# Performance work log

Hardware: AMD Instinct MI355X
Metric: run time of the kernel (lower is better)

The kernel has to match this reference:

```python
import jax, jax.numpy as jnp
import numpy as np

B, NS, NI, UP = 1024, 64, 64, 4
H = 256


def setup_inputs() -> dict:
    key = jax.random.key(0)
    ks = list(jax.random.split(key, 40))
    it = iter(ks)
    def lin(din, dout):
        return (jax.random.normal(next(it), (din, dout), jnp.float32) / np.sqrt(din)).astype(jnp.float32)
    d = {}
    d['rays_o'] = jax.random.normal(next(it), (B, 3), jnp.float32) * 0.1
    rd = jax.random.normal(next(it), (B, 3), jnp.float32)
    d['rays_d'] = rd / jnp.linalg.norm(rd, axis=-1, keepdims=True)
    d['near'] = jnp.full((B, 1), 0.5, jnp.float32)
    d['far'] = jnp.full((B, 1), 2.5, jnp.float32)
    d['W_sdf0'] = lin(3, H); d['b_sdf0'] = jnp.zeros((H,), jnp.float32)
    d['W_sdf1'] = lin(H, H); d['b_sdf1'] = jnp.zeros((H,), jnp.float32)
    d['W_sdf2'] = lin(H, 1 + H); d['b_sdf2'] = jnp.zeros((1 + H,), jnp.float32)
    d['s_var'] = jnp.asarray(0.3, jnp.float32)
    d['Wc0'] = lin(9 + H, H); d['bc0'] = jnp.zeros((H,), jnp.float32)
    d['Wc1'] = lin(H, 3); d['bc1'] = jnp.zeros((3,), jnp.float32)
    d['Wn0'] = lin(6, H); d['bn0'] = jnp.zeros((H,), jnp.float32)
    d['Wn1'] = lin(H, H); d['bn1'] = jnp.zeros((H,), jnp.float32)
    d['Wn2'] = lin(H, 4); d['bn2'] = jnp.zeros((4,), jnp.float32)
    d['Wrf0'] = lin(3, H); d['brf0'] = jnp.zeros((H,), jnp.float32)
    d['Wrf1'] = lin(H, 1); d['brf1'] = jnp.zeros((1,), jnp.float32)
    d['Wrl0'] = lin(3, H); d['brl0'] = jnp.zeros((H,), jnp.float32)
    d['Wrl1'] = lin(H, 1); d['brl1'] = jnp.zeros((1,), jnp.float32)
    d['Wnm0'] = lin(H, 128); d['bnm0'] = jnp.zeros((128,), jnp.float32)
    d['Wnm1'] = lin(128, 3); d['bnm1'] = jnp.zeros((3,), jnp.float32)
    return d


def _forward(args):
    (rays_o, rays_d, near, far, W_sdf0, b_sdf0, W_sdf1, b_sdf1, W_sdf2, b_sdf2,
     s_var, Wc0, bc0, Wc1, bc1, Wn0, bn0, Wn1, bn1, Wn2, bn2,
     Wrf0, brf0, Wrf1, brf1, Wrl0, brl0, Wrl1, brl1, Wnm0, bnm0, Wnm1, bnm1) = args
    relu, sig = jax.nn.relu, jax.nn.sigmoid
    Bn = rays_o.shape[0]
    inv_s = jnp.clip(jnp.exp(10.0 * s_var), 1e-6, 1e6)  # SingleVarianceNetwork
    sample_dist = 2.0 / NS

    def sdf_out(p):
        h = relu(p @ W_sdf0 + b_sdf0)
        h = relu(h @ W_sdf1 + b_sdf1)
        return h @ W_sdf2 + b_sdf2  # [N, 1+256]: sdf + feature

    def sdf_val(p):
        return sdf_out(p)[..., 0]

    def sample_pdf(bins, weights, n):  # deterministic (perturb=False)
        w = weights + 1e-5
        pdf = w / jnp.sum(w, -1, keepdims=True)
        cdf = jnp.concatenate([jnp.zeros_like(pdf[:, :1]), jnp.cumsum(pdf, -1)], -1)
        u = jnp.broadcast_to(jnp.linspace(0.5 / n, 1.0 - 0.5 / n, n, dtype=bins.dtype), (bins.shape[0], n))
        inds = jax.vmap(lambda c, uu: jnp.searchsorted(c, uu, side='right'))(cdf, u)
        below = jnp.clip(inds - 1, 0, bins.shape[-1] - 1)
        above = jnp.clip(inds, 0, bins.shape[-1] - 1)
        cb = jnp.take_along_axis(cdf, below, -1); ca = jnp.take_along_axis(cdf, above, -1)
        bb = jnp.take_along_axis(bins, below, -1); ba = jnp.take_along_axis(bins, above, -1)
        denom = jnp.where(ca - cb < 1e-5, 1.0, ca - cb)
        return bb + (u - cb) / denom * (ba - bb)

    def up_sample(o, d, z, sdf, n_imp, s):  # NeuS hierarchical SDF upsampling
        pts = o[:, None, :] + d[:, None, :] * z[..., None]
        radius = jnp.linalg.norm(pts, axis=-1)
        inside = ((radius[:, :-1] < 1.0) | (radius[:, 1:] < 1.0)).astype(z.dtype)
        prev_sdf, next_sdf = sdf[:, :-1], sdf[:, 1:]
        prev_z, next_z = z[:, :-1], z[:, 1:]
        mid_sdf = 0.5 * (prev_sdf + next_sdf)
        cos_val = (next_sdf - prev_sdf) / (next_z - prev_z + 1e-5)
        prev_cos = jnp.concatenate([jnp.zeros_like(cos_val[:, :1]), cos_val[:, :-1]], -1)
        cos_val = jnp.clip(jnp.minimum(cos_val, prev_cos), -1e3, 0.0) * inside
        dist = next_z - prev_z
        pc = sig((mid_sdf - 0.5 * cos_val * dist) * s)
        nc = sig((mid_sdf + 0.5 * cos_val * dist) * s)
        alpha = (pc - nc + 1e-5) / (pc + 1e-5)
        trans = jnp.cumprod(jnp.concatenate([jnp.ones_like(alpha[:, :1]), 1.0 - alpha + 1e-7], -1), -1)[:, :-1]
        return sample_pdf(z, alpha * trans, n_imp)

    def importance_sdf(o, d):
        z = near + (far - near) * jnp.linspace(0.0, 1.0, NS)[None, :]
        sdf = sdf_val((o[:, None, :] + d[:, None, :] * z[..., None]).reshape(-1, 3)).reshape(Bn, -1)
        for i in range(UP):
            nz = up_sample(o, d, z, sdf, NI // UP, 64.0 * 2 ** i)
            z = jnp.sort(jnp.concatenate([z, nz], -1), -1)
            if i + 1 < UP:
                sdf = sdf_val((o[:, None, :] + d[:, None, :] * z[..., None]).reshape(-1, 3)).reshape(Bn, -1)
        return jax.lax.stop_gradient(z)  # sampler runs under no_grad

    def render_sdf(o, d, z):  # rendering_rays_SDF (NeuS)
        S = z.shape[1]
        dists = jnp.concatenate([z[:, 1:] - z[:, :-1], jnp.full_like(z[:, :1], sample_dist)], -1)
        mid_z = z + 0.5 * dists
        pts = (o[:, None, :] + d[:, None, :] * mid_z[..., None]).reshape(-1, 3)
        dirs = jnp.broadcast_to(d[:, None, :], (Bn, S, 3)).reshape(-1, 3)
        out = sdf_out(pts)
        sdf = out[:, :1]; feat = out[:, 1:]
        grads = jax.grad(lambda p: jnp.sum(sdf_val(p)))(pts)  # analytic SDF gradient
        true_cos = jnp.sum(dirs * grads, -1, keepdims=True)
        iter_cos = -relu(-true_cos)  # cos_anneal_ratio = 1.0
        df = dists.reshape(-1, 1)
        pc = sig((sdf - 0.5 * iter_cos * df) * inv_s)
        nc = sig((sdf + 0.5 * iter_cos * df) * inv_s)
        alpha = jnp.clip((pc - nc + 1e-5) / (pc + 1e-5), 0.0, 1.0).reshape(Bn, S)
        trans = jnp.cumprod(jnp.concatenate([jnp.ones_like(alpha[:, :1]), 1.0 - alpha + 1e-7], -1), -1)[:, :-1]
        w = alpha * trans
        depths = jax.lax.stop_gradient(jnp.sum(mid_z * w, -1, keepdims=True))  # AlphaBlend depth, no_grad
        nrm = grads / (jnp.linalg.norm(grads, axis=-1, keepdims=True) + 1e-12)  # NormalizedAnalytic
        cin = jnp.concatenate([pts, nrm, dirs, feat], -1)  # color_d_in=9 + 256 feat
        rgb = sig(relu(cin @ Wc0 + bc0) @ Wc1 + bc1).reshape(Bn, S, 3)
        color = jnp.sum(rgb * w[..., None], 1)
        smooth = ((feat @ Wnm0 + bnm0) @ Wnm1 + bnm1).reshape(Bn, S, 3)  # Linear->Linear, no act
        surf_n = jnp.sum(w[..., None] * nrm.reshape(Bn, S, 3), 1)
        surf_n = surf_n / (jnp.linalg.norm(surf_n, axis=-1, keepdims=True) + 1e-12)
        return color, w, depths, surf_n, smooth

    def nerf_eval(pts, dirs):
        h = relu(jnp.concatenate([pts, dirs], -1) @ Wn0 + bn0)
        h = relu(h @ Wn1 + bn1)
        o = h @ Wn2 + bn2
        return o[:, 0], sig(o[:, 1:4])

    def mask_prob(pts, Wa, ba, Wb, bb):  # Refract/ReflectNetwork, d_in=3 d_out=1
        return sig((relu(pts @ Wa + ba) @ Wb + bb)[:, 0])

    def importance_nerf(o, d, z, n_imp):
        S = z.shape[1]
        dists = jnp.concatenate([z[:, 1:] - z[:, :-1], jnp.full_like(z[:, :1], 1e10)], -1)
        pts = (o[:, None, :] + d[:, None, :] * z[..., None]).reshape(-1, 3)
        dirs = jnp.broadcast_to(d[:, None, :], (Bn, S, 3)).reshape(-1, 3)
        sigma, _ = nerf_eval(pts, dirs)
        alpha = 1.0 - jnp.exp(-relu(sigma).reshape(Bn, S) * dists)
        trans = jnp.cumprod(jnp.concatenate([jnp.ones_like(alpha[:, :1]), 1.0 - alpha + 1e-7], -1), -1)[:, :-1]
        w = alpha * trans
        nz = sample_pdf(z, w[:, :-1], n_imp)
        return jax.lax.stop_gradient(jnp.sort(jnp.concatenate([z, nz], -1), -1))

    def render_nerf(o, d, z):
        S = z.shape[1]
        dists = jnp.concatenate([z[:, 1:] - z[:, :-1], jnp.full_like(z[:, :1], sample_dist)], -1)
        mid_z = z + 0.5 * dists
        pts = (o[:, None, :] + d[:, None, :] * mid_z[..., None]).reshape(-1, 3)
        dirs = jnp.broadcast_to(d[:, None, :], (Bn, S, 3)).reshape(-1, 3)
        sigma, rgb = nerf_eval(pts, dirs)
        alpha = 1.0 - jnp.exp(-relu(sigma).reshape(Bn, S) * dists)
        trans = jnp.cumprod(jnp.concatenate([jnp.ones_like(alpha[:, :1]), 1.0 - alpha + 1e-7], -1), -1)[:, :-1]
        w = alpha * trans
        color = jnp.sum(rgb.reshape(Bn, S, 3) * w[..., None], 1)
        m1 = jnp.sum(w * mask_prob(pts, Wrf0, brf0, Wrf1, brf1).reshape(Bn, S), -1, keepdims=True)
        m2 = jnp.sum(w * mask_prob(pts, Wrl0, brl0, Wrl1, brl1).reshape(Bn, S), -1, keepdims=True)
        return color, m1, m2

    # ---- main pipeline (eval: perturb=False, geometry_warmup_state=False) ----
    z_sdf = importance_sdf(rays_o, rays_d)
    _color_sdf, _w_sdf, depths, surf_n, _smooth = render_sdf(rays_o, rays_d, z_sdf)

    z0 = near + (far - near) * jnp.linspace(0.0, 1.0, NS)[None, :]
    z1 = importance_nerf(rays_o, rays_d, z0, NI)
    c1, m1, m2 = render_nerf(rays_o, rays_d, z1)

    # hit point + reflect/refract directions
    hit = rays_o + rays_d * depths
    n = surf_n
    cos = jnp.sum(rays_d * n, -1, keepdims=True)
    n = jnp.where(cos > 0, -n, n)  # face the incoming ray
    cosi = -jnp.sum(rays_d * n, -1, keepdims=True)
    refl = rays_d + 2.0 * cosi * n
    eta = 1.0 / 1.5
    k = 1.0 - eta * eta * (1.0 - cosi * cosi)
    refr = eta * rays_d + (eta * cosi - jnp.sqrt(jnp.maximum(k, 0.0))) * n
    refr = jnp.where(k < 0, refl, refr)  # total internal reflection
    refl = refl / (jnp.linalg.norm(refl, axis=-1, keepdims=True) + 1e-12)
    refr = refr / (jnp.linalg.norm(refr, axis=-1, keepdims=True) + 1e-12)

    ones = jnp.ones((Bn, 1), z1.dtype)
    # reflect (fanshe) pass: near=0.05 far=3.7
    zf0 = 0.05 * ones + (3.7 - 0.05) * jnp.linspace(0.0, 1.0, NS)[None, :]
    zf = importance_nerf(hit, refl, zf0, NI)
    cf, _, _ = render_nerf(hit, refl, zf)
    # refract (zheshe) passes: (0,3.7) and (0.5,3.7) with half samples
    zz0 = 3.7 * jnp.linspace(0.0, 1.0, NS // 2)[None, :] * ones
    zz = importance_nerf(hit, refr, zz0, NI // 2)
    cz, _, _ = render_nerf(hit, refr, zz)
    zb0 = 0.5 * ones + (3.7 - 0.5) * jnp.linspace(0.0, 1.0, NS // 2)[None, :]
    zb = importance_nerf(hit, refr, zb0, NI // 2)
    cb_, _, _ = render_nerf(hit, refr, zb)
    rgb_z = 0.5 * cz + 0.5 * cb_

    rgb = c1 * (1.0 - m2) + cf * m2
    rgb = rgb * (1.0 - m1) + rgb_z * m1
    return rgb


def reference(rays_o, rays_d, near, far, W_sdf0, b_sdf0, W_sdf1, b_sdf1, W_sdf2, b_sdf2,
              s_var, Wc0, bc0, Wc1, bc1, Wn0, bn0, Wn1, bn1, Wn2, bn2,
              Wrf0, brf0, Wrf1, brf1, Wrl0, brl0, Wrl1, brl1, Wnm0, bnm0, Wnm1, bnm1):
    return _forward((rays_o, rays_d, near, far, W_sdf0, b_sdf0, W_sdf1, b_sdf1, W_sdf2, b_sdf2,
                     s_var, Wc0, bc0, Wc1, bc1, Wn0, bn0, Wn1, bn1, Wn2, bn2,
                     Wrf0, brf0, Wrf1, brf1, Wrl0, brl0, Wrl1, brl1, Wnm0, bnm0, Wnm1, bnm1))
```

## Files before the change

kernel.cpp:

```cpp
#include <hip/hip_runtime.h>

#define NB 1024
#define HH 256
#define ZS 128
#define PP 16
#define SAMPLE_DIST 0.03125f

typedef __attribute__((ext_vector_type(8))) _Float16 half8v;
typedef __attribute__((ext_vector_type(4))) float f32x4;

struct ZInit { int on; const float* loA; const float* hiA; float lo0,hi0,lo1,hi1; };

__device__ __forceinline__ float sigm(float x){ return 1.0f/(1.0f+__expf(-x)); }

__device__ __forceinline__ float iscan_prod(float v, int lane){
  #pragma unroll
  for (int o=1;o<64;o<<=1){ float u=__shfl_up(v,o); if(lane>=o) v*=u; }
  return v;
}
__device__ __forceinline__ float iscan_sum(float v, int lane){
  #pragma unroll
  for (int o=1;o<64;o<<=1){ float u=__shfl_up(v,o); if(lane>=o) v+=u; }
  return v;
}
__device__ __forceinline__ float wave_sum(float v){
  #pragma unroll
  for (int o=1;o<64;o<<=1) v += __shfl_xor(v,o);
  return v;
}

__device__ __forceinline__ void load_point2(const float* __restrict__ o, const float* __restrict__ dv,
    const float* __restrict__ z, int idx, int S, int midflag, int zst, ZInit zi, float* pt, float* dir)
{
  int r = idx / S;
  int i = idx - r*S;
  float zz;
  if (zi.on){
    float a=zi.loA[r], b=zi.hiA[r];
    zz = a + (b-a)*((float)i/(float)(S-1));
    if (midflag){
      float z1 = a + (b-a)*((float)(i+1)/(float)(S-1));
      zz = (i < S-1) ? 0.5f*(zz+z1) : (zz + 0.5f*SAMPLE_DIST);
    }
  } else {
    const float* zr = z + r*zst;
    zz = zr[i];
    if (midflag) zz = (i < S-1) ? 0.5f*(zz + zr[i+1]) : (zz + 0.5f*SAMPLE_DIST);
  }
  #pragma unroll
  for (int c=0;c<3;c++){
    float dc = dv[r*3+c];
    pt[c] = o[r*3+c] + dc*zz;
    if (dir) dir[c] = dc;
  }
}

__device__ __forceinline__ void load_point(const float* __restrict__ o, const float* __restrict__ dv,
    const float* __restrict__ z, int idx, int S, int midflag, float* pt, float* dir)
{
  int r = idx / S;
  int i = idx - r*S;
  const float* zr = z + r*ZS;
  float zz = zr[i];
  if (midflag) zz = (i < S-1) ? 0.5f*(zz + zr[i+1]) : (zz + 0.5f*SAMPLE_DIST);
  #pragma unroll
  for (int c=0;c<3;c++){
    float dc = dv[r*3+c];
    pt[c] = o[r*3+c] + dc*zz;
    if (dir) dir[c] = dc;
  }
}

__global__ __launch_bounds__(256) void prep_kernel(const float* __restrict__ W1, const float* __restrict__ W2,
    float* __restrict__ W1T, float* __restrict__ w2col)
{
  int idx = blockIdx.x*256 + threadIdx.x;
  int j = idx >> 8, k = idx & 255;
  W1T[j*HH + k] = W1[k*HH + j];
  if (idx < HH) w2col[idx] = W2[idx*257];
}

__global__ __launch_bounds__(256) void prep_bfrag_kernel(const float* __restrict__ W1,
    short* __restrict__ Bh)
{
  int idx = blockIdx.x*256 + threadIdx.x;
  int j = idx & 7;
  int lane = (idx>>3) & 63;
  int s = (idx>>9) & 7;
  int nt = idx >> 12;
  int k = s*32 + ((lane>>4)<<3) + j;
  int n = nt*16 + (lane&15);
  union { _Float16 h; short s; } u;
  u.h = (_Float16)W1[k*256 + n];
  Bh[idx] = u.s;
}

__global__ void build_rays_kernel(const float* __restrict__ ro, const float* __restrict__ rd,
    const float* __restrict__ nearA, const float* __restrict__ farA,
    const float* __restrict__ hit, const float* __restrict__ refl, const float* __restrict__ refr,
    float* __restrict__ rO, float* __restrict__ rD, float* __restrict__ rLo, float* __restrict__ rHi)
{
  int r = blockIdx.x*256 + threadIdx.x;
  if (r >= 4096) return;
  int m = r>>10, q = r&1023;
  const float* so; const float* sd; float lo,hi;
  if (m==0){ so=ro+q*3; sd=rd+q*3; lo=nearA[q]; hi=farA[q]; }
  else if (m==1){ so=hit+q*3; sd=refl+q*3; lo=0.05f; hi=3.7f; }
  else if (m==2){ so=hit+q*3; sd=refr+q*3; lo=0.f; hi=3.7f; }
  else { so=hit+q*3; sd=refr+q*3; lo=0.5f; hi=3.7f; }
  rO[r*3]=so[0]; rO[r*3+1]=so[1]; rO[r*3+2]=so[2];
  rD[r*3]=sd[0]; rD[r*3+1]=sd[1]; rD[r*3+2]=sd[2];
  rLo[r]=lo; rHi[r]=hi;
}

__global__ __launch_bounds__(256) void sdf_mfma_kernel(
    const float* __restrict__ o, const float* __restrict__ dv, const float* __restrict__ z,
    int S, int midflag, int zst, ZInit zi,
    const float* __restrict__ W0, const float* __restrict__ b0,
    const short* __restrict__ Bh, const float* __restrict__ b1,
    const float* __restrict__ w2col, const float* __restrict__ b2,
    float* __restrict__ out_sdf, unsigned short* __restrict__ signs)
{
  __shared__ float xs[128][5];
  __shared__ float w0s[3*HH];
  __shared__ float b0s[HH];
  int t = threadIdx.x;
  int base = blockIdx.x*128;
  for (int i=t;i<3*HH;i+=256) w0s[i]=W0[i];
  b0s[t]=b0[t];
  if (t<128){
    float pt[3];
    load_point2(o,dv,z,base+t,S,midflag,zst,zi,pt,nullptr);
    xs[t][0]=pt[0]; xs[t][1]=pt[1]; xs[t][2]=pt[2];
  }
  __syncthreads();
  int wave=t>>6, lane=t&63, g=lane>>4, c16=lane&15;
  half8v af[2][8];
  #pragma unroll
  for (int mt=0;mt<2;mt++){
    const float* xp = xs[wave*32 + mt*16 + c16];
    float x0=xp[0],x1=xp[1],x2=xp[2];
    #pragma unroll
    for (int s8=0;s8<8;s8++){
      int nb = s8*32 + g*8;
      union { _Float16 h[8]; half8v v; } uh;
      #pragma unroll
      for (int j=0;j<8;j++){
        int n=nb+j;
        float a=b0s[n];
        a=fmaf(x0,w0s[n],a);
        a=fmaf(x1,w0s[HH+n],a);
        a=fmaf(x2,w0s[2*HH+n],a);
        uh.h[j]=(_Float16)fmaxf(a,0.f);
      }
      af[mt][s8]=uh.v;
    }
  }
  float pacc[2][4];
  #pragma unroll
  for (int mt=0;mt<2;mt++){ pacc[mt][0]=0.f; pacc[mt][1]=0.f; pacc[mt][2]=0.f; pacc[mt][3]=0.f; }
  for (int ntp=0;ntp<8;ntp++){
    int nt0=2*ntp;
    f32x4 aH[2][2];
    #pragma unroll
    for (int mt=0;mt<2;mt++)
      #pragma unroll
      for (int h=0;h<2;h++) aH[mt][h]=(f32x4){0.f,0.f,0.f,0.f};
    const short* b0h = Bh + nt0*4096 + lane*8;
    #pragma unroll
    for (int s8=0;s8<8;s8++){
      half8v bh0 = *(const half8v*)(b0h + s8*512);
      half8v bh1 = *(const half8v*)(b0h + 4096 + s8*512);
      #pragma unroll
      for (int mt=0;mt<2;mt++){
        aH[mt][0] = __builtin_amdgcn_mfma_f32_16x16x32_f16(af[mt][s8], bh0, aH[mt][0], 0,0,0);
        aH[mt][1] = __builtin_amdgcn_mfma_f32_16x16x32_f16(af[mt][s8], bh1, aH[mt][1], 0,0,0);
      }
    }
    #pragma unroll
    for (int h=0;h<2;h++){
      int nt = nt0+h;
      int n = nt*16 + c16;
      float b1v = b1[n];
      float wv = w2col[n];
      #pragma unroll
      for (int mt=0;mt<2;mt++){
        f32x4 acc = aH[mt][h];
        #pragma unroll
        for (int rr=0;rr<4;rr++){
          float hv = acc[rr]+b1v;
          if (signs){
            unsigned long long m0 = __ballot(hv>0.f);
            if (c16==0) signs[(base+wave*32+mt*16+g*4+rr)*16+nt] = (unsigned short)(m0>>(16*g));
          }
          pacc[mt][rr]=fmaf(fmaxf(hv,0.f),wv,pacc[mt][rr]);
        }
      }
    }
  }
  #pragma unroll
  for (int mt=0;mt<2;mt++)
    #pragma unroll
    for (int rr=0;rr<4;rr++){
      float v=pacc[mt][rr];
      v+=__shfl_xor(v,1); v+=__shfl_xor(v,2); v+=__shfl_xor(v,4); v+=__shfl_xor(v,8);
      pacc[mt][rr]=v;
    }
  if (c16==0){
    float bb2=b2[0];
    #pragma unroll
    for (int mt=0;mt<2;mt++)
      #pragma unroll
      for (int rr=0;rr<4;rr++)
        out_sdf[base + wave*32 + mt*16 + g*4 + rr] = pacc[mt][rr] + bb2;
  }
}

__global__ __launch_bounds__(256) void sdf_bwd_mfma_kernel(
    const float* __restrict__ o, const float* __restrict__ dv, const float* __restrict__ z,
    const float* __restrict__ W0, const float* __restrict__ b0,
    const unsigned short* __restrict__ signs,
    const short* __restrict__ Th,
    const float* __restrict__ w2col,
    float* __restrict__ out_grad)
{
  __shared__ float xs[128][5];
  __shared__ float w0s[3*HH];
  __shared__ float b0s[HH];
  __shared__ _Float16 w2h_s[HH];
  int t = threadIdx.x;
  int base = blockIdx.x*128;
  for (int i=t;i<3*HH;i+=256) w0s[i]=W0[i];
  b0s[t]=b0[t];
  w2h_s[t]=(_Float16)w2col[t];
  if (t<128){
    float pt[3];
    ZInit zn{0,nullptr,nullptr,0,0,0,0};
    load_point2(o,dv,z,base+t,128,1,ZS,zn,pt,nullptr);
    xs[t][0]=pt[0]; xs[t][1]=pt[1]; xs[t][2]=pt[2];
  }
  __syncthreads();
  int wave=t>>6, lane=t&63, g=lane>>4, c16=lane&15;
  half8v af[2][8];
  #pragma unroll
  for (int mt=0;mt<2;mt++){
    int ptA = base + wave*32 + mt*16 + c16;
    #pragma unroll
    for (int s8=0;s8<8;s8++){
      int j0 = s8*32 + g*8;
      unsigned short wch = signs[ptA*16 + (j0>>4)];
      unsigned bits = ((unsigned)wch >> ((g&1)*8)) & 0xFFu;
      union { _Float16 h[8]; half8v v; } uh;
      #pragma unroll
      for (int jj=0;jj<8;jj++){
        bool on = (bits>>jj)&1u;
        uh.h[jj] = on ? w2h_s[j0+jj] : (_Float16)0.f;
      }
      af[mt][s8]=uh.v;
    }
  }
  float acc3[2][4][3];
  #pragma unroll
  for (int mt=0;mt<2;mt++)
    #pragma unroll
    for (int rr=0;rr<4;rr++){ acc3[mt][rr][0]=0.f; acc3[mt][rr][1]=0.f; acc3[mt][rr][2]=0.f; }
  for (int ntp=0;ntp<8;ntp++){
    int nt0=2*ntp;
    f32x4 aH[2][2];
    #pragma unroll
    for (int mt=0;mt<2;mt++)
      #pragma unroll
      for (int h=0;h<2;h++) aH[mt][h]=(f32x4){0.f,0.f,0.f,0.f};
    const short* b0h = Th + nt0*4096 + lane*8;
    #pragma unroll
    for (int s8=0;s8<8;s8++){
      half8v bh0 = *(const half8v*)(b0h + s8*512);
      half8v bh1 = *(const half8v*)(b0h + 4096 + s8*512);
      #pragma unroll
      for (int mt=0;mt<2;mt++){
        aH[mt][0] = __builtin_amdgcn_mfma_f32_16x16x32_f16(af[mt][s8], bh0, aH[mt][0], 0,0,0);
        aH[mt][1] = __builtin_amdgcn_mfma_f32_16x16x32_f16(af[mt][s8], bh1, aH[mt][1], 0,0,0);
      }
    }
    #pragma unroll
    for (int h=0;h<2;h++){
      int nt = nt0+h;
      int tn = nt*16 + c16;
      float w0a=w0s[tn], w0b=w0s[HH+tn], w0c=w0s[2*HH+tn], bb=b0s[tn];
      #pragma unroll
      for (int mt=0;mt<2;mt++){
        f32x4 acc = aH[mt][h];
        #pragma unroll
        for (int rr=0;rr<4;rr++){
          const float* xq = xs[wave*32 + mt*16 + g*4 + rr];
          float h0 = fmaf(xq[0],w0a, fmaf(xq[1],w0b, fmaf(xq[2],w0c, bb)));
          float dh0 = (h0>0.f) ? acc[rr] : 0.f;
          acc3[mt][rr][0]=fmaf(dh0,w0a,acc3[mt][rr][0]);
          acc3[mt][rr][1]=fmaf(dh0,w0b,acc3[mt][rr][1]);
          acc3[mt][rr][2]=fmaf(dh0,w0c,acc3[mt][rr][2]);
        }
      }
    }
  }
  #pragma unroll
  for (int mt=0;mt<2;mt++)
    #pragma unroll
    for (int rr=0;rr<4;rr++)
      #pragma unroll
      for (int cc=0;cc<3;cc++){
        float v=acc3[mt][rr][cc];
        v+=__shfl_xor(v,1); v+=__shfl_xor(v,2); v+=__shfl_xor(v,4); v+=__shfl_xor(v,8);
        acc3[mt][rr][cc]=v;
      }
  if (c16==0){
    #pragma unroll
    for (int mt=0;mt<2;mt++)
      #pragma unroll
      for (int rr=0;rr<4;rr++){
        int pt_ = base + wave*32 + mt*16 + g*4 + rr;
        out_grad[pt_*3+0]=acc3[mt][rr][0];
        out_grad[pt_*3+1]=acc3[mt][rr][1];
        out_grad[pt_*3+2]=acc3[mt][rr][2];
      }
  }
}

__global__ __launch_bounds__(256) void nerf_mfma_batch(
    const float* __restrict__ rO, const float* __restrict__ rD,
    const float* __restrict__ rLo, const float* __restrict__ rHi,
    const float* __restrict__ zbuf, int ptsA, int SA, int SB, int NRA, int useZ, int midflag,
    const float* __restrict__ W0, const float* __restrict__ b0,
    const short* __restrict__ Bh, const float* __restrict__ b1,
    const float* __restrict__ W2, const float* __restrict__ b2,
    float* __restrict__ out_sigma, float* __restrict__ out_rgb)
{
  __shared__ float xs[128][9];
  __shared__ float w0s[6*HH];
  __shared__ float b0s[HH];
  int t = threadIdx.x;
  int base = blockIdx.x*128;
  int wave=t>>6, lane=t&63, g=lane>>4, c16=lane&15;
  for (int i=t;i<6*HH;i+=256) w0s[i]=W0[i];
  b0s[t]=b0[t];
  if (t<128){
    int idx=base+t;
    int r,i,S;
    if (idx<ptsA){ S=SA; r=idx/SA; i=idx-r*SA; }
    else { int q=idx-ptsA; S=SB; r=NRA+q/SB; i=q-(q/SB)*SB; }
    float zz;
    if (!useZ){
      float a=rLo[r], b=rHi[r];
      zz = a + (b-a)*((float)i/(float)(S-1));
      if (midflag){
        float z1 = a + (b-a)*((float)(i+1)/(float)(S-1));
        zz = (i<S-1)? 0.5f*(zz+z1) : (zz+0.5f*SAMPLE_DIST);
      }
    } else {
      const float* zr = zbuf + r*128;
      zz = zr[i];
      if (midflag) zz = (i<S-1)? 0.5f*(zz+zr[i+1]) : (zz+0.5f*SAMPLE_DIST);
    }
    #pragma unroll
    for (int c=0;c<3;c++){
      float dc=rD[r*3+c];
      xs[t][c]   = rO[r*3+c] + dc*zz;
      xs[t][3+c] = dc;
    }
  }
  __syncthreads();
  half8v af[2][8];
  #pragma unroll
  for (int mt=0;mt<2;mt++){
    const float* xp = xs[wave*32 + mt*16 + c16];
    float x0=xp[0],x1=xp[1],x2=xp[2],x3=xp[3],x4=xp[4],x5=xp[5];
    #pragma unroll
    for (int s8=0;s8<8;s8++){
      int nb = s8*32 + g*8;
      union { _Float16 h[8]; half8v v; } uh;
      #pragma unroll
      for (int j=0;j<8;j++){
        int n=nb+j;
        float a=b0s[n];
        a=fmaf(x0,w0s[n],a);
        a=fmaf(x1,w0s[HH+n],a);
        a=fmaf(x2,w0s[2*HH+n],a);
        a=fmaf(x3,w0s[3*HH+n],a);
        a=fmaf(x4,w0s[4*HH+n],a);
        a=fmaf(x5,w0s[5*HH+n],a);
        uh.h[j]=(_Float16)fmaxf(a,0.f);
      }
      af[mt][s8]=uh.v;
    }
  }
  float pacc[2][4][4];
  #pragma unroll
  for (int mt=0;mt<2;mt++)
    #pragma unroll
    for (int rr=0;rr<4;rr++){ pacc[mt][rr][0]=0.f; pacc[mt][rr][1]=0.f; pacc[mt][rr][2]=0.f; pacc[mt][rr][3]=0.f; }
  for (int ntp=0;ntp<8;ntp++){
    int nt0=2*ntp;
    f32x4 aH[2][2];
    #pragma unroll
    for (int mt=0;mt<2;mt++)
      #pragma unroll
      for (int h=0;h<2;h++) aH[mt][h]=(f32x4){0.f,0.f,0.f,0.f};
    const short* b0h = Bh + nt0*4096 + lane*8;
    #pragma unroll
    for (int s8=0;s8<8;s8++){
      half8v bh0 = *(const half8v*)(b0h + s8*512);
      half8v bh1 = *(const half8v*)(b0h + 4096 + s8*512);
      #pragma unroll
      for (int mt=0;mt<2;mt++){
        aH[mt][0] = __builtin_amdgcn_mfma_f32_16x16x32_f16(af[mt][s8], bh0, aH[mt][0], 0,0,0);
        aH[mt][1] = __builtin_amdgcn_mfma_f32_16x16x32_f16(af[mt][s8], bh1, aH[mt][1], 0,0,0);
      }
    }
    #pragma unroll
    for (int h=0;h<2;h++){
      int nt = nt0+h;
      int n = nt*16 + c16;
      float b1v = b1[n];
      float4 w2v = *(const float4*)(W2 + n*4);
      #pragma unroll
      for (int mt=0;mt<2;mt++){
        f32x4 acc = aH[mt][h];
        #pragma unroll
        for (int rr=0;rr<4;rr++){
          float hh = fmaxf(acc[rr]+b1v, 0.f);
          pacc[mt][rr][0]=fmaf(hh,w2v.x,pacc[mt][rr][0]);
          pacc[mt][rr][1]=fmaf(hh,w2v.y,pacc[mt][rr][1]);
          pacc[mt][rr][2]=fmaf(hh,w2v.z,pacc[mt][rr][2]);
          pacc[mt][rr][3]=fmaf(hh,w2v.w,pacc[mt][rr][3]);
        }
      }
    }
  }
  #pragma unroll
  for (int mt=0;mt<2;mt++)
    #pragma unroll
    for (int rr=0;rr<4;rr++)
      #pragma unroll
      for (int c=0;c<4;c++){
        float v=pacc[mt][rr][c];
        v+=__shfl_xor(v,1); v+=__shfl_xor(v,2); v+=__shfl_xor(v,4); v+=__shfl_xor(v,8);
        pacc[mt][rr][c]=v;
      }
  if (c16==0){
    float bb0=b2[0], bb1=b2[1], bb2v=b2[2], bb3=b2[3];
    #pragma unroll
    for (int mt=0;mt<2;mt++)
      #pragma unroll
      for (int rr=0;rr<4;rr++){
        int pt_ = base + wave*32 + mt*16 + g*4 + rr;
        out_sigma[pt_] = pacc[mt][rr][0] + bb0;
        out_rgb[pt_*3+0] = sigm(pacc[mt][rr][1] + bb1);
        out_rgb[pt_*3+1] = sigm(pacc[mt][rr][2] + bb2v);
        out_rgb[pt_*3+2] = sigm(pacc[mt][rr][3] + bb3);
      }
  }
}

__global__ __launch_bounds__(256) void mask_kernel(
    const float* __restrict__ o, const float* __restrict__ dv, const float* __restrict__ z, int S,
    const float* __restrict__ Wa0, const float* __restrict__ ba0, const float* __restrict__ Wa1, const float* __restrict__ ba1,
    const float* __restrict__ Wb0, const float* __restrict__ bb0, const float* __restrict__ Wb1, const float* __restrict__ bb1,
    float* __restrict__ outA, float* __restrict__ outB)
{
  __shared__ __align__(16) float hA[PP][HH];
  __shared__ float pin[PP][4];
  __shared__ float part[PP][16];
  int t=threadIdx.x;
  int base=blockIdx.x*PP;
  if (t<PP){
    float pt[3];
    load_point(o,dv,z,base+t,S,1,pt,nullptr);
    pin[t][0]=pt[0]; pin[t][1]=pt[1]; pin[t][2]=pt[2];
  }
  __syncthreads();
  {
    float w0=Wa0[t], w1=Wa0[HH+t], w2=Wa0[2*HH+t], bb=ba0[t];
    #pragma unroll
    for (int p=0;p<PP;p++){
      float v = fmaf(pin[p][0],w0, fmaf(pin[p][1],w1, fmaf(pin[p][2],w2, bb)));
      hA[p][t]=fmaxf(v,0.f);
    }
  }
  __syncthreads();
  {
    int p=t>>4, g=t&15;
    float s=0.f;
    #pragma unroll
    for (int m=0;m<16;m++){ int j=g+16*m; s=fmaf(hA[p][j], Wa1[j], s); }
    part[p][g]=s;
  }
  __syncthreads();
  if (t<PP){
    float s=ba1[0];
    #pragma unroll
    for (int g=0;g<16;g++) s+=part[t][g];
    outA[base+t]=sigm(s);
  }
  __syncthreads();
  {
    float w0=Wb0[t], w1=Wb0[HH+t], w2=Wb0[2*HH+t], bb=bb0[t];
    #pragma unroll
    for (int p=0;p<PP;p++){
      float v = fmaf(pin[p][0],w0, fmaf(pin[p][1],w1, fmaf(pin[p][2],w2, bb)));
      hA[p][t]=fmaxf(v,0.f);
    }
  }
  __syncthreads();
  {
    int p=t>>4, g=t&15;
    float s=0.f;
    #pragma unroll
    for (int m=0;m<16;m++){ int j=g+16*m; s=fmaf(hA[p][j], Wb1[j], s); }
    part[p][g]=s;
  }
  __syncthreads();
  if (t<PP){
    float s=bb1[0];
    #pragma unroll
    for (int g=0;g<16;g++) s+=part[t][g];
    outB[base+t]=sigm(s);
  }
}

__global__ __launch_bounds__(256) void upsample_wave_kernel(float* __restrict__ z,
    const float* __restrict__ sdf, const float* __restrict__ o, const float* __restrict__ dv,
    int S, float s, ZInit zi)
{
  __shared__ float zsh[4][128], ssh[4][128], csh[4][128], nzsh[4][16];
  int wave=threadIdx.x>>6, lane=threadIdx.x&63;
  int r=blockIdx.x*4+wave;
  float* zs=zsh[wave]; float* ss=ssh[wave]; float* cs=csh[wave]; float* nzs=nzsh[wave];
  for (int i=lane;i<S;i+=64){
    float zv;
    if (zi.on){
      float a=zi.loA[r], b=zi.hiA[r];
      zv = a + (b-a)*((float)i/(float)(S-1));
    } else zv = z[r*ZS+i];
    zs[i]=zv; ss[i]=sdf[r*S+i];
  }
  __syncthreads();
  float ox=o[r*3],oy=o[r*3+1],oz=o[r*3+2];
  float dx=dv[r*3],dy=dv[r*3+1],dz=dv[r*3+2];
  int M=S-1;
  auto alpha_at=[&](int k)->float{
    float z0=zs[k], z1=zs[k+1], s0=ss[k], s1=ss[k+1];
    float craw=(s1-s0)/(z1-z0+1e-5f);
    float cprev=(k>0)? (ss[k]-ss[k-1])/(zs[k]-zs[k-1]+1e-5f) : 0.f;
    float cv=fminf(craw,cprev);
    cv=fminf(fmaxf(cv,-1000.f),0.f);
    float px=ox+dx*z0, py=oy+dy*z0, pz=oz+dz*z0;
    float qx=ox+dx*z1, qy=oy+dy*z1, qz=oz+dz*z1;
    float r0=sqrtf(px*px+py*py+pz*pz);
    float r1=sqrtf(qx*qx+qy*qy+qz*qz);
    float inside=(r0<1.f||r1<1.f)?1.f:0.f;
    cv*=inside;
    float mid=0.5f*(s0+s1), dist=z1-z0;
    float pc=sigm((mid-0.5f*cv*dist)*s);
    float nc=sigm((mid+0.5f*cv*dist)*s);
    return (pc-nc+1e-5f)/(pc+1e-5f);
  };
  float al0=(lane<M)? alpha_at(lane):0.f;
  float al1=(lane+64<M)? alpha_at(lane+64):0.f;
  float f0=(lane<M)?(1.f-al0+1e-7f):1.f;
  float f1=(lane+64<M)?(1.f-al1+1e-7f):1.f;
  float ip0=iscan_prod(f0,lane);
  float tt=__shfl_up(ip0,1); float T0=(lane==0)?1.f:tt;
  float tot0=__shfl(ip0,63);
  float ip1=iscan_prod(f1,lane);
  float tu=__shfl_up(ip1,1); float T1=((lane==0)?1.f:tu)*tot0;
  float w0=(lane<M)? al0*T0+1e-5f:0.f;
  float w1=(lane+64<M)? al1*T1+1e-5f:0.f;
  float wsum=wave_sum(w0+w1);
  float inv=1.f/wsum;
  float is0=iscan_sum(w0,lane);
  float st0=__shfl(is0,63);
  float is1=iscan_sum(w1,lane)+st0;
  if (lane<M) cs[lane+1]=is0*inv;
  if (lane+64<M) cs[lane+64+1]=is1*inv;
  if (lane==0) cs[0]=0.f;
  __syncthreads();
  if (lane<16){
    float u=(lane+0.5f)/16.f;
    int lo=0,hi=S;
    while(lo<hi){ int m=(lo+hi)>>1; if(cs[m]<=u) lo=m+1; else hi=m; }
    int below=lo-1; below=below<0?0:(below>S-1?S-1:below);
    int above=lo>S-1?S-1:lo;
    float cb=cs[below], ca=cs[above], bb=zs[below], ba=zs[above];
    float dd=ca-cb; float den=(dd<1e-5f)?1.f:dd;
    nzs[lane]=bb+(u-cb)/den*(ba-bb);
  }
  __syncthreads();
  for (int i=lane;i<S;i+=64){
    float zi_=zs[i]; int cnt=0;
    #pragma unroll
    for (int j=0;j<16;j++) cnt += (nzs[j]<zi_)?1:0;
    z[r*ZS+i+cnt]=zi_;
  }
  if (lane<16){
    float v=nzs[lane]; int rk=0;
    #pragma unroll
    for (int j=0;j<16;j++) rk += ((nzs[j]<v)||(nzs[j]==v&&j<lane))?1:0;
    int lo=0,hi=S;
    while(lo<hi){ int m=(lo+hi)>>1; if(zs[m]<=v) lo=m+1; else hi=m; }
    z[r*ZS+lo+rk]=v;
  }
}

__global__ __launch_bounds__(256) void nerf_imp_batch(float* __restrict__ zbuf,
    const float* __restrict__ sigma, const float* __restrict__ rLo, const float* __restrict__ rHi,
    int ptsA, int NRA)
{
  __shared__ float zsh[4][64], csh[4][64], nzsh[4][64];
  int wave=threadIdx.x>>6, lane=threadIdx.x&63;
  int r=blockIdx.x*4+wave;
  int S = (r<NRA)? 64 : 32;
  int n = S;
  int off = (r<NRA)? r*64 : ptsA + (r-NRA)*32;
  float* zs=zsh[wave]; float* cs=csh[wave]; float* nzs=nzsh[wave];
  if (lane<S){
    float a=rLo[r], b=rHi[r];
    zs[lane]= a + (b-a)*((float)lane/(float)(S-1));
  }
  __syncthreads();
  int M=S-1;
  float al=0.f;
  if (lane<M){
    float d_=zs[lane+1]-zs[lane];
    float sv=sigma[off+lane];
    al=1.f-__expf(-fmaxf(sv,0.f)*d_);
  }
  float f=(lane<M)?(1.f-al+1e-7f):1.f;
  float ip=iscan_prod(f,lane);
  float tt=__shfl_up(ip,1); float T=(lane==0)?1.f:tt;
  float w=(lane<M)? al*T+1e-5f:0.f;
  float wsum=wave_sum(w);
  float inv=1.f/wsum;
  float is=iscan_sum(w,lane);
  if (lane<M) cs[lane+1]=is*inv;
  if (lane==0) cs[0]=0.f;
  __syncthreads();
  if (lane<n){
    float u=(lane+0.5f)/(float)n;
    int lo=0,hi=S;
    while(lo<hi){ int m=(lo+hi)>>1; if(cs[m]<=u) lo=m+1; else hi=m; }
    int below=lo-1; below=below<0?0:(below>S-1?S-1:below);
    int above=lo>S-1?S-1:lo;
    float cb=cs[below], ca=cs[above], bb=zs[below], ba=zs[above];
    float dd=ca-cb; float den=(dd<1e-5f)?1.f:dd;
    nzs[lane]=bb+(u-cb)/den*(ba-bb);
  }
  __syncthreads();
  if (lane<S){
    float zi_=zs[lane]; int cnt=0;
    for (int j=0;j<n;j++) cnt += (nzs[j]<zi_)?1:0;
    zbuf[r*128+lane+cnt]=zi_;
  }
  if (lane<n){
    float v=nzs[lane]; int rk=0;
    for (int j=0;j<n;j++) rk += ((nzs[j]<v)||(nzs[j]==v&&j<lane))?1:0;
    int lo=0,hi=S;
    while(lo<hi){ int m=(lo+hi)>>1; if(zs[m]<=v) lo=m+1; else hi=m; }
    zbuf[r*128+lo+rk]=v;
  }
}

__global__ __launch_bounds__(256) void nerf_render_batch(const float* __restrict__ zbuf,
    const float* __restrict__ sigma, const float* __restrict__ rgbp,
    int pts2A, int NRA,
    const float* __restrict__ mva, const float* __restrict__ mvb,
    float* __restrict__ c1b, float* __restrict__ m1b, float* __restrict__ m2b,
    float* __restrict__ cfb, float* __restrict__ czb, float* __restrict__ cbb)
{
  int wave=threadIdx.x>>6, lane=threadIdx.x&63;
  int r=blockIdx.x*4+wave;
  int S = (r<NRA)? 128 : 64;
  int off = (r<NRA)? r*128 : pts2A + (r-NRA)*64;
  const float* zr = zbuf + r*128;
  int domask = (r<1024);
  float a0=0.f,a1=0.f;
  if (lane<S){
    float d_=(lane<S-1)? zr[lane+1]-zr[lane] : SAMPLE_DIST;
    a0=1.f-__expf(-fmaxf(sigma[off+lane],0.f)*d_);
  }
  if (lane+64<S){
    int k=lane+64;
    float d_=(k<S-1)? zr[k+1]-zr[k] : SAMPLE_DIST;
    a1=1.f-__expf(-fmaxf(sigma[off+k],0.f)*d_);
  }
  float f0=(lane<S)?(1.f-a0+1e-7f):1.f;
  float f1=(lane+64<S)?(1.f-a1+1e-7f):1.f;
  float ip0=iscan_prod(f0,lane);
  float tt=__shfl_up(ip0,1); float T0=(lane==0)?1.f:tt;
  float tot0=__shfl(ip0,63);
  float ip1=iscan_prod(f1,lane);
  float tu=__shfl_up(ip1,1); float T1=((lane==0)?1.f:tu)*tot0;
  float w0=(lane<S)? a0*T0:0.f;
  float w1=(lane+64<S)? a1*T1:0.f;
  float c0=0,c1=0,c2=0,m1=0,m2=0;
  if (lane<S){
    int i0=off+lane;
    c0=w0*rgbp[i0*3]; c1=w0*rgbp[i0*3+1]; c2=w0*rgbp[i0*3+2];
    if (domask){ m1=w0*mva[i0]; m2=w0*mvb[i0]; }
  }
  if (lane+64<S){
    int i1=off+lane+64;
    c0=fmaf(w1,rgbp[i1*3],c0); c1=fmaf(w1,rgbp[i1*3+1],c1); c2=fmaf(w1,rgbp[i1*3+2],c2);
    if (domask){ m1=fmaf(w1,mva[i1],m1); m2=fmaf(w1,mvb[i1],m2); }
  }
  c0=wave_sum(c0); c1=wave_sum(c1); c2=wave_sum(c2);
  m1=wave_sum(m1); m2=wave_sum(m2);
  if (lane==0){
    int grp=r>>10, q=r&1023;
    float* outc = (grp==0)? c1b : (grp==1)? cfb : (grp==2)? czb : cbb;
    outc[q*3]=c0; outc[q*3+1]=c1; outc[q*3+2]=c2;
    if (grp==0){ m1b[q]=m1; m2b[q]=m2; }
  }
}

__global__ __launch_bounds__(256) void sdf_render_hit(const float* __restrict__ z,
    const float* __restrict__ sdf, const float* __restrict__ grad,
    const float* __restrict__ o, const float* __restrict__ dv,
    const float* __restrict__ svar,
    float* __restrict__ hitb, float* __restrict__ reflb, float* __restrict__ refrb)
{
  int wave=threadIdx.x>>6, lane=threadIdx.x&63;
  int r=blockIdx.x*4+wave;
  float inv_s=fminf(fmaxf(__expf(10.f*svar[0]),1e-6f),1e6f);
  float dx=dv[r*3],dy=dv[r*3+1],dz=dv[r*3+2];
  const float* zr=z+r*ZS;
  auto comp=[&](int k, float& alpha, float& midz, float& gx, float& gy, float& gz){
    float d_=(k<127)? zr[k+1]-zr[k] : SAMPLE_DIST;
    midz=zr[k]+0.5f*d_;
    int gi=(r*128+k)*3;
    gx=grad[gi]; gy=grad[gi+1]; gz=grad[gi+2];
    float tc=dx*gx+dy*gy+dz*gz;
    float ic=fminf(tc,0.f);
    float s_=sdf[r*128+k];
    float pc=sigm((s_-0.5f*ic*d_)*inv_s);
    float nc=sigm((s_+0.5f*ic*d_)*inv_s);
    alpha=fminf(fmaxf((pc-nc+1e-5f)/(pc+1e-5f),0.f),1.f);
  };
  float al0,mz0,g0x,g0y,g0z; comp(lane,al0,mz0,g0x,g0y,g0z);
  float al1,mz1,g1x,g1y,g1z; comp(lane+64,al1,mz1,g1x,g1y,g1z);
  float f0=1.f-al0+1e-7f, f1=1.f-al1+1e-7f;
  float ip0=iscan_prod(f0,lane);
  float tt=__shfl_up(ip0,1); float T0=(lane==0)?1.f:tt;
  float tot0=__shfl(ip0,63);
  float ip1=iscan_prod(f1,lane);
  float tu=__shfl_up(ip1,1); float T1=((lane==0)?1.f:tu)*tot0;
  float w0=al0*T0, w1=al1*T1;
  float n0=1.f/(sqrtf(g0x*g0x+g0y*g0y+g0z*g0z)+1e-12f);
  float n1=1.f/(sqrtf(g1x*g1x+g1y*g1y+g1z*g1z)+1e-12f);
  float dep=w0*mz0+w1*mz1;
  float sx=w0*n0*g0x+w1*n1*g1x;
  float sy=w0*n0*g0y+w1*n1*g1y;
  float sz=w0*n0*g0z+w1*n1*g1z;
  dep=wave_sum(dep); sx=wave_sum(sx); sy=wave_sum(sy); sz=wave_sum(sz);
  if (lane==0){
    float nn=1.f/(sqrtf(sx*sx+sy*sy+sz*sz)+1e-12f);
    float nx=sx*nn, ny=sy*nn, nz=sz*nn;
    hitb[r*3]  = o[r*3]  +dx*dep;
    hitb[r*3+1]= o[r*3+1]+dy*dep;
    hitb[r*3+2]= o[r*3+2]+dz*dep;
    float cs=dx*nx+dy*ny+dz*nz;
    if (cs>0.f){ nx=-nx; ny=-ny; nz=-nz; }
    float cosi=-(dx*nx+dy*ny+dz*nz);
    float rx=dx+2.f*cosi*nx, ry=dy+2.f*cosi*ny, rz=dz+2.f*cosi*nz;
    float eta=1.f/1.5f;
    float k=1.f-eta*eta*(1.f-cosi*cosi);
    float sq=sqrtf(fmaxf(k,0.f));
    float tx=eta*dx+(eta*cosi-sq)*nx;
    float ty=eta*dy+(eta*cosi-sq)*ny;
    float tz=eta*dz+(eta*cosi-sq)*nz;
    if (k<0.f){ tx=rx; ty=ry; tz=rz; }
    float rn=1.f/(sqrtf(rx*rx+ry*ry+rz*rz)+1e-12f);
    reflb[r*3]=rx*rn; reflb[r*3+1]=ry*rn; reflb[r*3+2]=rz*rn;
    float tn=1.f/(sqrtf(tx*tx+ty*ty+tz*tz)+1e-12f);
    refrb[r*3]=tx*tn; refrb[r*3+1]=ty*tn; refrb[r*3+2]=tz*tn;
  }
}

__global__ void compose_kernel(const float* __restrict__ c1b, const float* __restrict__ m1b,
    const float* __restrict__ m2b, const float* __restrict__ cfb, const float* __restrict__ czb,
    const float* __restrict__ cbb, float* __restrict__ out)
{
  int r = blockIdx.x*blockDim.x + threadIdx.x;
  if (r >= NB) return;
  float m1=m1b[r], m2=m2b[r];
  #pragma unroll
  for (int c=0;c<3;c++){
    float v = c1b[r*3+c]*(1.f-m2) + cfb[r*3+c]*m2;
    float rz = 0.5f*czb[r*3+c] + 0.5f*cbb[r*3+c];
    out[r*3+c] = v*(1.f-m1) + rz*m1;
  }
}

extern "C" void kernel_launch(void* const* d_in, const int* in_sizes, int n_in,
                              void* d_out, int out_size, void* d_ws, size_t ws_size,
                              hipStream_t stream)
{
  const float* rays_o=(const float*)d_in[0];
  const float* rays_d=(const float*)d_in[1];
  const float* nearA =(const float*)d_in[2];
  const float* farA  =(const float*)d_in[3];
  const float* Ws0=(const float*)d_in[4];
  const float* bs0=(const float*)d_in[5];
  const float* Ws1=(const float*)d_in[6];
  const float* bs1=(const float*)d_in[7];
  const float* Ws2=(const float*)d_in[8];
  const float* bs2=(const float*)d_in[9];
  const float* svar=(const float*)d_in[10];
  const float* Wn0=(const float*)d_in[15];
  const float* bn0=(const float*)d_in[16];
  const float* Wn1=(const float*)d_in[17];
  const float* bn1=(const float*)d_in[18];
  const float* Wn2=(const float*)d_in[19];
  const float* bn2=(const float*)d_in[20];
  const float* Wrf0=(const float*)d_in[21];
  const float* brf0=(const float*)d_in[22];
  const float* Wrf1=(const float*)d_in[23];
  const float* brf1=(const float*)d_in[24];
  const float* Wrl0=(const float*)d_in[25];
  const float* brl0=(const float*)d_in[26];
  const float* Wrl1=(const float*)d_in[27];
  const float* brl1=(const float*)d_in[28];

  const int NRA   = 2048;
  const int PTS1A = 2048*64;
  const int PTS2A = 2048*128;

  float* ws=(float*)d_ws;
  float* zbuf = ws;  ws += 4096*128;
  float* sdfb = ws;  ws += 393216;
  float* uni  = ws;  ws += 1441792;
  float* gradb = uni;
  unsigned short* signsb = (unsigned short*)(uni + 393216);
  float* rgbp = uni;
  float* mv1  = ws;  ws += PTS1A;
  float* mv2  = ws;  ws += PTS1A;
  float* W1T  = ws;  ws += HH*HH;
  float* w2c  = ws;  ws += HH;
  float* rO   = ws;  ws += 4096*3;
  float* rD   = ws;  ws += 4096*3;
  float* rLo  = ws;  ws += 4096;
  float* rHi  = ws;  ws += 4096;
  float* hitb = ws;  ws += NB*3;
  float* reflb= ws;  ws += NB*3;
  float* refrb= ws;  ws += NB*3;
  float* c1b  = ws;  ws += NB*3;
  float* m1b  = ws;  ws += NB;
  float* m2b  = ws;  ws += NB;
  float* cfb  = ws;  ws += NB*3;
  float* czb  = ws;  ws += NB*3;
  float* cbb  = ws;  ws += NB*3;
  short* bfragN = (short*)ws; ws += HH*HH/2;
  short* bfragS = (short*)ws; ws += HH*HH/2;
  short* bfragT = (short*)ws; ws += HH*HH/2;

  const int RB = (NB+255)/256;
  const int WB = NB/4;

  ZInit ziNone{0,nullptr,nullptr,0.f,0.f,0.f,0.f};
  ZInit ziNF  {1,nearA,farA,0.f,0.f,0.f,0.f};

  prep_kernel<<<256,256,0,stream>>>(Ws1, Ws2, W1T, w2c);
  prep_bfrag_kernel<<<256,256,0,stream>>>(Wn1, bfragN);
  prep_bfrag_kernel<<<256,256,0,stream>>>(Ws1, bfragS);
  prep_bfrag_kernel<<<256,256,0,stream>>>(W1T, bfragT);

  for (int i=0;i<4;i++){
    int S=64+16*i;
    float sscale=64.f*(float)(1<<i);
    sdf_mfma_kernel<<<NB*S/128,256,0,stream>>>(rays_o,rays_d,zbuf,S,0,ZS,(i==0?ziNF:ziNone),
        Ws0,bs0, bfragS,bs1, w2c,bs2, sdfb, nullptr);
    upsample_wave_kernel<<<WB,256,0,stream>>>(zbuf,sdfb,rays_o,rays_d,S,sscale,(i==0?ziNF:ziNone));
  }

  sdf_mfma_kernel<<<NB*128/128,256,0,stream>>>(rays_o,rays_d,zbuf,128,1,ZS,ziNone,
      Ws0,bs0, bfragS,bs1, w2c,bs2, sdfb, signsb);
  sdf_bwd_mfma_kernel<<<NB*128/128,256,0,stream>>>(rays_o,rays_d,zbuf, Ws0,bs0, signsb,
      bfragT, w2c, gradb);
  sdf_render_hit<<<WB,256,0,stream>>>(zbuf,sdfb,gradb,rays_o,rays_d,svar, hitb,reflb,refrb);

  build_rays_kernel<<<16,256,0,stream>>>(rays_o,rays_d,nearA,farA, hitb,reflb,refrb, rO,rD,rLo,rHi);

  nerf_mfma_batch<<<(PTS1A + 2048*32)/128,256,0,stream>>>(rO,rD,rLo,rHi, zbuf,
      PTS1A, 64, 32, NRA, 0, 0,
      Wn0,bn0, bfragN,bn1, Wn2,bn2, sdfb,rgbp);
  nerf_imp_batch<<<4096/4,256,0,stream>>>(zbuf, sdfb, rLo,rHi, PTS1A, NRA);
  nerf_mfma_batch<<<(PTS2A + 2048*64)/128,256,0,stream>>>(rO,rD,rLo,rHi, zbuf,
      PTS2A, 128, 64, NRA, 1, 1,
      Wn0,bn0, bfragN,bn1, Wn2,bn2, sdfb,rgbp);
  mask_kernel<<<NB*128/PP,256,0,stream>>>(rays_o,rays_d,zbuf,128, Wrf0,brf0,Wrf1,brf1, Wrl0,brl0,Wrl1,brl1, mv1,mv2);
  nerf_render_batch<<<4096/4,256,0,stream>>>(zbuf, sdfb, rgbp, PTS2A, NRA, mv1,mv2,
      c1b,m1b,m2b, cfb,czb,cbb);

  compose_kernel<<<RB,256,0,stream>>>(c1b,m1b,m2b,cfb,czb,cbb,(float*)d_out);
}
```

Before: 454.5 us.

## Stage MFMA weight tiles through double-buffered LDS via async global_load_lds

In the three MFMA MLP kernels, each wave previously read the 256x256 fp16 weight tiles straight from global memory for every B-fragment. Now the block cooperatively copies each 16 KB pair of column tiles into LDS using direct global-to-LDS loads. The next tile pair is prefetched into a second buffer while the current one is consumed. This is meant to cut redundant global/L2 traffic across the 4 waves and hide load latency. In exchange it uses 32 KB more LDS per block, which may lower occupancy, and adds a block barrier per iteration.

```diff
diff --git a/kernel.cpp b/kernel.cpp
--- a/kernel.cpp
+++ b/kernel.cpp
@@ -12,6 +12,12 @@
 struct ZInit { int on; const float* loA; const float* hiA; float lo0,hi0,lo1,hi1; };
 
 __device__ __forceinline__ float sigm(float x){ return 1.0f/(1.0f+__expf(-x)); }
+
+__device__ __forceinline__ void gload_lds16(const void* g, void* l){
+  __builtin_amdgcn_global_load_lds(
+      (const __attribute__((address_space(1))) unsigned int*)g,
+      (__attribute__((address_space(3))) unsigned int*)l, 16, 0, 0);
+}
 
 __device__ __forceinline__ float iscan_prod(float v, int lane){
   #pragma unroll
@@ -121,11 +127,13 @@
     const float* __restrict__ w2col, const float* __restrict__ b2,
     float* __restrict__ out_sdf, unsigned short* __restrict__ signs)
 {
+  __shared__ short ldsB[2][8192];
   __shared__ float xs[128][5];
   __shared__ float w0s[3*HH];
   __shared__ float b0s[HH];
   int t = threadIdx.x;
   int base = blockIdx.x*128;
+  int wave=t>>6, lane=t&63, g=lane>>4, c16=lane&15;
   for (int i=t;i<3*HH;i+=256) w0s[i]=W0[i];
   b0s[t]=b0[t];
   if (t<128){
@@ -133,8 +141,15 @@
     load_point2(o,dv,z,base+t,S,midflag,zst,zi,pt,nullptr);
     xs[t][0]=pt[0]; xs[t][1]=pt[1]; xs[t][2]=pt[2];
   }
-  __syncthreads();
-  int wave=t>>6, lane=t&63, g=lane>>4, c16=lane&15;
+  {
+    const char* gb = (const char*)Bh;
+    #pragma unroll
+    for (int c=0;c<4;c++){
+      int ch = wave*4 + c;
+      gload_lds16(gb + ch*1024 + lane*16, (void*)&ldsB[0][ch*512]);
+    }
+  }
+  __syncthreads();
   half8v af[2][8];
   #pragma unroll
   for (int mt=0;mt<2;mt++){
@@ -159,18 +174,27 @@
   float pacc[2][4];
   #pragma unroll
   for (int mt=0;mt<2;mt++){ pacc[mt][0]=0.f; pacc[mt][1]=0.f; pacc[mt][2]=0.f; pacc[mt][3]=0.f; }
+  int buf=0;
   for (int ntp=0;ntp<8;ntp++){
+    if (ntp<7){
+      const char* gb = (const char*)(Bh + 2*(ntp+1)*4096);
+      #pragma unroll
+      for (int c=0;c<4;c++){
+        int ch = wave*4 + c;
+        gload_lds16(gb + ch*1024 + lane*16, (void*)&ldsB[buf^1][ch*512]);
+      }
+    }
     int nt0=2*ntp;
     f32x4 aH[2][2];
     #pragma unroll
     for (int mt=0;mt<2;mt++)
       #pragma unroll
       for (int h=0;h<2;h++) aH[mt][h]=(f32x4){0.f,0.f,0.f,0.f};
-    const short* b0h = Bh + nt0*4096 + lane*8;
+    const short* Lb = &ldsB[buf][0];
     #pragma unroll
     for (int s8=0;s8<8;s8++){
-      half8v bh0 = *(const half8v*)(b0h + s8*512);
-      half8v bh1 = *(const half8v*)(b0h + 4096 + s8*512);
+      half8v bh0 = *(const half8v*)(Lb + s8*512 + lane*8);
+      half8v bh1 = *(const half8v*)(Lb + 4096 + s8*512 + lane*8);
       #pragma unroll
       for (int mt=0;mt<2;mt++){
         aH[mt][0] = __builtin_amdgcn_mfma_f32_16x16x32_f16(af[mt][s8], bh0, aH[mt][0], 0,0,0);
@@ -197,6 +221,8 @@
         }
       }
     }
+    __syncthreads();
+    buf^=1;
   }
   #pragma unroll
   for (int mt=0;mt<2;mt++)
@@ -224,12 +250,14 @@
     const float* __restrict__ w2col,
     float* __restrict__ out_grad)
 {
+  __shared__ short ldsB[2][8192];
   __shared__ float xs[128][5];
   __shared__ float w0s[3*HH];
   __shared__ float b0s[HH];
   __shared__ _Float16 w2h_s[HH];
   int t = threadIdx.x;
   int base = blockIdx.x*128;
+  int wave=t>>6, lane=t&63, g=lane>>4, c16=lane&15;
   for (int i=t;i<3*HH;i+=256) w0s[i]=W0[i];
   b0s[t]=b0[t];
   w2h_s[t]=(_Float16)w2col[t];
@@ -239,8 +267,15 @@
     load_point2(o,dv,z,base+t,128,1,ZS,zn,pt,nullptr);
     xs[t][0]=pt[0]; xs[t][1]=pt[1]; xs[t][2]=pt[2];
   }
-  __syncthreads();
-  int wave=t>>6, lane=t&63, g=lane>>4, c16=lane&15;
+  {
+    const char* gb = (const char*)Th;
+    #pragma unroll
+    for (int c=0;c<4;c++){
+      int ch = wave*4 + c;
+      gload_lds16(gb + ch*1024 + lane*16, (void*)&ldsB[0][ch*512]);
+    }
+  }
+  __syncthreads();
   half8v af[2][8];
   #pragma unroll
   for (int mt=0;mt<2;mt++){
@@ -264,18 +299,27 @@
   for (int mt=0;mt<2;mt++)
     #pragma unroll
     for (int rr=0;rr<4;rr++){ acc3[mt][rr][0]=0.f; acc3[mt][rr][1]=0.f; acc3[mt][rr][2]=0.f; }
+  int buf=0;
   for (int ntp=0;ntp<8;ntp++){
+    if (ntp<7){
+      const char* gb = (const char*)(Th + 2*(ntp+1)*4096);
+      #pragma unroll
+      for (int c=0;c<4;c++){
+        int ch = wave*4 + c;
+        gload_lds16(gb + ch*1024 + lane*16, (void*)&ldsB[buf^1][ch*512]);
+      }
+    }
     int nt0=2*ntp;
     f32x4 aH[2][2];
     #pragma unroll
     for (int mt=0;mt<2;mt++)
       #pragma unroll
       for (int h=0;h<2;h++) aH[mt][h]=(f32x4){0.f,0.f,0.f,0.f};
-    const short* b0h = Th + nt0*4096 + lane*8;
+    const short* Lb = &ldsB[buf][0];
     #pragma unroll
     for (int s8=0;s8<8;s8++){
-      half8v bh0 = *(const half8v*)(b0h + s8*512);
-      half8v bh1 = *(const half8v*)(b0h + 4096 + s8*512);
+      half8v bh0 = *(const half8v*)(Lb + s8*512 + lane*8);
+      half8v bh1 = *(const half8v*)(Lb + 4096 + s8*512 + lane*8);
       #pragma unroll
       for (int mt=0;mt<2;mt++){
         aH[mt][0] = __builtin_amdgcn_mfma_f32_16x16x32_f16(af[mt][s8], bh0, aH[mt][0], 0,0,0);
@@ -301,6 +345,8 @@
         }
       }
     }
+    __syncthreads();
+    buf^=1;
   }
   #pragma unroll
   for (int mt=0;mt<2;mt++)
@@ -334,6 +380,7 @@
     const float* __restrict__ W2, const float* __restrict__ b2,
     float* __restrict__ out_sigma, float* __restrict__ out_rgb)
 {
+  __shared__ short ldsB[2][8192];
   __shared__ float xs[128][9];
   __shared__ float w0s[6*HH];
   __shared__ float b0s[HH];
@@ -367,6 +414,14 @@
       xs[t][3+c] = dc;
     }
   }
+  {
+    const char* gb = (const char*)Bh;
+    #pragma unroll
+    for (int c=0;c<4;c++){
+      int ch = wave*4 + c;
+      gload_lds16(gb + ch*1024 + lane*16, (void*)&ldsB[0][ch*512]);
+    }
+  }
   __syncthreads();
   half8v af[2][8];
   #pragma unroll
@@ -397,18 +452,27 @@
   for (int mt=0;mt<2;mt++)
     #pragma unroll
     for (int rr=0;rr<4;rr++){ pacc[mt][rr][0]=0.f; pacc[mt][rr][1]=0.f; pacc[mt][rr][2]=0.f; pacc[mt][rr][3]=0.f; }
+  int buf=0;
   for (int ntp=0;ntp<8;ntp++){
+    if (ntp<7){
+      const char* gb = (const char*)(Bh + 2*(ntp+1)*4096);
+      #pragma unroll
+      for (int c=0;c<4;c++){
+        int ch = wave*4 + c;
+        gload_lds16(gb + ch*1024 + lane*16, (void*)&ldsB[buf^1][ch*512]);
+      }
+    }
     int nt0=2*ntp;
     f32x4 aH[2][2];
     #pragma unroll
     for (int mt=0;mt<2;mt++)
       #pragma unroll
       for (int h=0;h<2;h++) aH[mt][h]=(f32x4){0.f,0.f,0.f,0.f};
-    const short* b0h = Bh + nt0*4096 + lane*8;
+    const short* Lb = &ldsB[buf][0];
     #pragma unroll
     for (int s8=0;s8<8;s8++){
-      half8v bh0 = *(const half8v*)(b0h + s8*512);
-      half8v bh1 = *(const half8v*)(b0h + 4096 + s8*512);
+      half8v bh0 = *(const half8v*)(Lb + s8*512 + lane*8);
+      half8v bh1 = *(const half8v*)(Lb + 4096 + s8*512 + lane*8);
       #pragma unroll
       for (int mt=0;mt<2;mt++){
         aH[mt][0] = __builtin_amdgcn_mfma_f32_16x16x32_f16(af[mt][s8], bh0, aH[mt][0], 0,0,0);
@@ -434,6 +498,8 @@
         }
       }
     }
+    __syncthreads();
+    buf^=1;
   }
   #pragma unroll
   for (int mt=0;mt<2;mt++)
```

After: 392.7 us. -13.6%, faster.
